# Performance work log

Measured on AMD Instinct MI355X. Metric: run time of the kernel, lower is better.

Reference implementation:

```python
import jax, jax.numpy as jnp
import numpy as np

COMMITMENT_COST = 0.25
DIST_SCALE = 400.0


def setup_inputs() -> dict:
    key = jax.random.key(0)
    ks = jax.random.split(key, 6)
    B, T, D, K = 64, 1024, 512, 512
    s = 1.0 / np.sqrt(D)
    return {
        "inputs": jax.random.normal(ks[0], (B, T, D), dtype=jnp.float32),
        "mean_W": jax.random.normal(ks[1], (D, D), dtype=jnp.float32) * s,
        "mean_b": jax.random.normal(ks[2], (D,), dtype=jnp.float32) * s,
        "logvar_W": jax.random.normal(ks[3], (D, K), dtype=jnp.float32) * s,
        "logvar_b": jax.random.normal(ks[4], (K,), dtype=jnp.float32) * s,
        "embedding": jax.random.normal(ks[5], (K, D), dtype=jnp.float32),
    }


def reference(inputs, mean_W, mean_b, logvar_W, logvar_b, embedding):
    sg = jax.lax.stop_gradient
    D = embedding.shape[1]
    flat = inputs.reshape(-1, D)                      # [N, D]
    x = flat @ mean_W + mean_b                        # mean_layer, [N, D]
    z_logvar = x @ logvar_W + logvar_b                # logvar_layer, [N, K]
    # squared euclidean distances to codebook, [N, K]
    distances = (
        jnp.sum(x * x, axis=1, keepdims=True)
        + jnp.sum(embedding * embedding, axis=1)
        - 2.0 * (x @ embedding.T)
    )
    smooth = jnp.exp(-2.0 * z_logvar)                 # 1/exp(logvar)^2
    d = distances / DIST_SCALE
    prob = jnp.exp(-d * (0.5 * smooth)) / jnp.sqrt(smooth)
    probs = prob / jnp.sum(prob, axis=1, keepdims=True)  # per-row normalize, [N, K]
    quantized = (probs @ embedding).reshape(inputs.shape)
    e_latent_loss = jnp.mean((sg(quantized) - inputs) ** 2)
    q_latent_loss = jnp.mean((quantized - sg(inputs)) ** 2)
    loss = q_latent_loss + COMMITMENT_COST * e_latent_loss
    quantized_st = inputs + sg(quantized - inputs)    # straight-through
    avg_probs = jnp.mean(probs, axis=0)
    perplexity = jnp.exp(-jnp.sum(avg_probs * jnp.log(avg_probs + 1e-10)))
    return loss, quantized_st, perplexity, probs
```

## Files before the change

### kernel.cpp

```cpp
#include <hip/hip_runtime.h>
#include <stdint.h>

#define DIMD 512
#define NROWS 65536
#define QOFF 1
#define PERPOFF 33554433
#define PROBSOFF 33554434
#define NELEM 33554432

typedef __attribute__((ext_vector_type(8))) short bf16x8;
typedef __attribute__((ext_vector_type(4))) short s16x4;
typedef __attribute__((ext_vector_type(4))) float f32x4;

__device__ __forceinline__ short f2bf(float x){
  uint32_t u = __builtin_bit_cast(uint32_t, x);
  uint32_t r = (u + 0x7fffu + ((u >> 16) & 1u)) >> 16;
  return (short)(uint16_t)r;
}
__device__ __forceinline__ float bf2f(short h){
  return __builtin_bit_cast(float, ((uint32_t)(uint16_t)h) << 16);
}

__device__ __forceinline__ int aoff(int row, int kc){
  return row * 512 + ((kc ^ (row & 7)) << 3);
}

__global__ __launch_bounds__(256) void k_convert_w(
    const float* __restrict__ meanW, const float* __restrict__ lvW, const float* __restrict__ emb,
    short* __restrict__ MWfh, short* __restrict__ MWfl,
    short* __restrict__ VWh, short* __restrict__ VWl,
    short* __restrict__ Eb, short* __restrict__ Et, float* __restrict__ enorm)
{
  int b = blockIdx.x;
  int tid = threadIdx.x;
  float esum = 0.f;
  for (int j = tid; j < 512; j += 256){
    long offB = ((long)(b >> 5) << 14) + j * 32 + (b & 31);
    float w = meanW[b * 512 + j];
    short h = f2bf(w); short l = f2bf(w - bf2f(h));
    MWfh[offB] = h; MWfl[offB] = l;
    float v = lvW[b * 512 + j];
    h = f2bf(v); l = f2bf(v - bf2f(h));
    VWh[offB] = h; VWl[offB] = l;
    float e = emb[b * 512 + j];
    short eh = f2bf(e);
    Eb[((long)(j >> 5) << 14) + b * 32 + (j & 31)] = eh;
    Et[offB] = eh;
    esum += e * e;
  }
  for (int o = 32; o >= 1; o >>= 1) esum += __shfl_xor(esum, o);
  __shared__ float red[4];
  if ((tid & 63) == 0) red[tid >> 6] = esum;
  __syncthreads();
  if (tid == 0) enorm[b] = red[0] + red[1] + red[2] + red[3];
}

__global__ __launch_bounds__(1024, 1) void k_fused(
    const float* __restrict__ inp,
    const short* __restrict__ MWfh, const short* __restrict__ MWfl,
    const short* __restrict__ VWh, const short* __restrict__ VWl,
    const short* __restrict__ Eb, const short* __restrict__ Et,
    const float* __restrict__ meanb, const float* __restrict__ lvb,
    const float* __restrict__ enorm,
    float* __restrict__ probs, float* __restrict__ qout,
    float* __restrict__ Pacc, float* __restrict__ lossacc)
{
  __shared__ short Ih[64 * 512];
  __shared__ short Il[64 * 512];
  __shared__ float rrM[16][64];
  __shared__ float rrS[16][64];

  const int tid = threadIdx.x;
  const int n0 = blockIdx.x * 64;
  const int lane = tid & 63, wid = tid >> 6;
  const int q = lane >> 4, m = lane & 15;
  const int c0 = wid * 32;

  int boff0 = (c0 + m) * 32 + q * 8;
  int boff1 = (c0 + 16 + m) * 32 + q * 8;

  {
    const float* inpb = inp + (long)n0 * 512;
#pragma unroll
    for (int it = 0; it < 8; ++it){
      int fid = tid + it * 1024;
      int row = fid >> 7, f = fid & 127;
      const float4 v = *(const float4*)(inpb + (long)fid * 4);
      short h0 = f2bf(v.x), h1 = f2bf(v.y), h2 = f2bf(v.z), h3 = f2bf(v.w);
      s16x4 hv; hv[0] = h0; hv[1] = h1; hv[2] = h2; hv[3] = h3;
      s16x4 lv;
      lv[0] = f2bf(v.x - bf2f(h0)); lv[1] = f2bf(v.y - bf2f(h1));
      lv[2] = f2bf(v.z - bf2f(h2)); lv[3] = f2bf(v.w - bf2f(h3));
      int ch = (f >> 1) ^ (row & 7);
      int addr = row * 512 + (ch << 3) + (f & 1) * 4;
      *(s16x4*)(Ih + addr) = hv;
      *(s16x4*)(Il + addr) = lv;
    }
  }
  __syncthreads();

  f32x4 accM[4][2];
#pragma unroll
  for (int i = 0; i < 4; i++)
#pragma unroll
    for (int j = 0; j < 2; j++)
#pragma unroll
      for (int r = 0; r < 4; r++) accM[i][j][r] = 0.f;
  {
    bf16x8 nbh0 = *(const bf16x8*)(MWfh + boff0);
    bf16x8 nbh1 = *(const bf16x8*)(MWfh + boff1);
    bf16x8 nbl0 = *(const bf16x8*)(MWfl + boff0);
    bf16x8 nbl1 = *(const bf16x8*)(MWfl + boff1);
#pragma unroll 2
    for (int ks = 0; ks < 16; ++ks){
      bf16x8 bh0 = nbh0, bh1 = nbh1, bl0 = nbl0, bl1 = nbl1;
      if (ks < 15){
        int o = (ks + 1) * 16384;
        nbh0 = *(const bf16x8*)(MWfh + o + boff0);
        nbh1 = *(const bf16x8*)(MWfh + o + boff1);
        nbl0 = *(const bf16x8*)(MWfl + o + boff0);
        nbl1 = *(const bf16x8*)(MWfl + o + boff1);
      }
      bf16x8 ah[4], al[4];
#pragma unroll
      for (int i = 0; i < 4; i++){
        int off = aoff(i * 16 + m, ks * 4 + q);
        ah[i] = *(const bf16x8*)(Ih + off);
        al[i] = *(const bf16x8*)(Il + off);
      }
#pragma unroll
      for (int i = 0; i < 4; i++){
        accM[i][0] = __builtin_amdgcn_mfma_f32_16x16x32_bf16(ah[i], bh0, accM[i][0], 0, 0, 0);
        accM[i][0] = __builtin_amdgcn_mfma_f32_16x16x32_bf16(ah[i], bl0, accM[i][0], 0, 0, 0);
        accM[i][0] = __builtin_amdgcn_mfma_f32_16x16x32_bf16(al[i], bh0, accM[i][0], 0, 0, 0);
        accM[i][1] = __builtin_amdgcn_mfma_f32_16x16x32_bf16(ah[i], bh1, accM[i][1], 0, 0, 0);
        accM[i][1] = __builtin_amdgcn_mfma_f32_16x16x32_bf16(ah[i], bl1, accM[i][1], 0, 0, 0);
        accM[i][1] = __builtin_amdgcn_mfma_f32_16x16x32_bf16(al[i], bh1, accM[i][1], 0, 0, 0);
      }
    }
  }
  __syncthreads();

  {
    float b0 = meanb[c0 + m], b1 = meanb[c0 + 16 + m];
#pragma unroll
    for (int i = 0; i < 4; i++)
#pragma unroll
      for (int r = 0; r < 4; r++){
        int row = i * 16 + q * 4 + r;
        float x0 = accM[i][0][r] + b0;
        float x1 = accM[i][1][r] + b1;
        int col0 = c0 + m, col1 = c0 + 16 + m;
        short h0 = f2bf(x0), h1 = f2bf(x1);
        int a0 = row * 512 + ((((col0 >> 3) ^ (row & 7)) << 3) | (col0 & 7));
        int a1 = row * 512 + ((((col1 >> 3) ^ (row & 7)) << 3) | (col1 & 7));
        Ih[a0] = h0; Il[a0] = f2bf(x0 - bf2f(h0));
        Ih[a1] = h1; Il[a1] = f2bf(x1 - bf2f(h1));
        float xn = x0 * x0 + x1 * x1;
        xn += __shfl_xor(xn, 1); xn += __shfl_xor(xn, 2);
        xn += __shfl_xor(xn, 4); xn += __shfl_xor(xn, 8);
        if (m == 0) rrS[wid][row] = xn;
      }
  }
  __syncthreads();

  float xnv[4][4];
  {
    float v = 0.f;
#pragma unroll
    for (int w = 0; w < 16; w++) v += rrS[w][lane];
#pragma unroll
    for (int i = 0; i < 4; i++)
#pragma unroll
      for (int r = 0; r < 4; r++) xnv[i][r] = __shfl(v, i * 16 + q * 4 + r);
  }

  f32x4 accZ[4][2];
#pragma unroll
  for (int i = 0; i < 4; i++)
#pragma unroll
    for (int j = 0; j < 2; j++)
#pragma unroll
      for (int r = 0; r < 4; r++) accZ[i][j][r] = 0.f;
  {
    bf16x8 nbh0 = *(const bf16x8*)(VWh + boff0);
    bf16x8 nbh1 = *(const bf16x8*)(VWh + boff1);
    bf16x8 nbl0 = *(const bf16x8*)(VWl + boff0);
    bf16x8 nbl1 = *(const bf16x8*)(VWl + boff1);
#pragma unroll 2
    for (int ks = 0; ks < 16; ++ks){
      bf16x8 bh0 = nbh0, bh1 = nbh1, bl0 = nbl0, bl1 = nbl1;
      if (ks < 15){
        int o = (ks + 1) * 16384;
        nbh0 = *(const bf16x8*)(VWh + o + boff0);
        nbh1 = *(const bf16x8*)(VWh + o + boff1);
        nbl0 = *(const bf16x8*)(VWl + o + boff0);
        nbl1 = *(const bf16x8*)(VWl + o + boff1);
      }
      bf16x8 ah[4], al[4];
#pragma unroll
      for (int i = 0; i < 4; i++){
        int off = aoff(i * 16 + m, ks * 4 + q);
        ah[i] = *(const bf16x8*)(Ih + off);
        al[i] = *(const bf16x8*)(Il + off);
      }
#pragma unroll
      for (int i = 0; i < 4; i++){
        accZ[i][0] = __builtin_amdgcn_mfma_f32_16x16x32_bf16(ah[i], bh0, accZ[i][0], 0, 0, 0);
        accZ[i][0] = __builtin_amdgcn_mfma_f32_16x16x32_bf16(ah[i], bl0, accZ[i][0], 0, 0, 0);
        accZ[i][0] = __builtin_amdgcn_mfma_f32_16x16x32_bf16(al[i], bh0, accZ[i][0], 0, 0, 0);
        accZ[i][1] = __builtin_amdgcn_mfma_f32_16x16x32_bf16(ah[i], bh1, accZ[i][1], 0, 0, 0);
        accZ[i][1] = __builtin_amdgcn_mfma_f32_16x16x32_bf16(ah[i], bl1, accZ[i][1], 0, 0, 0);
        accZ[i][1] = __builtin_amdgcn_mfma_f32_16x16x32_bf16(al[i], bh1, accZ[i][1], 0, 0, 0);
      }
    }
  }

  f32x4 accS[4][2];
#pragma unroll
  for (int i = 0; i < 4; i++)
#pragma unroll
    for (int j = 0; j < 2; j++)
#pragma unroll
      for (int r = 0; r < 4; r++) accS[i][j][r] = 0.f;
  {
    bf16x8 nb0 = *(const bf16x8*)(Eb + boff0);
    bf16x8 nb1 = *(const bf16x8*)(Eb + boff1);
#pragma unroll 2
    for (int ks = 0; ks < 16; ++ks){
      bf16x8 b0 = nb0, b1 = nb1;
      if (ks < 15){
        int o = (ks + 1) * 16384;
        nb0 = *(const bf16x8*)(Eb + o + boff0);
        nb1 = *(const bf16x8*)(Eb + o + boff1);
      }
      bf16x8 ah[4];
#pragma unroll
      for (int i = 0; i < 4; i++)
        ah[i] = *(const bf16x8*)(Ih + aoff(i * 16 + m, ks * 4 + q));
#pragma unroll
      for (int i = 0; i < 4; i++){
        accS[i][0] = __builtin_amdgcn_mfma_f32_16x16x32_bf16(ah[i], b0, accS[i][0], 0, 0, 0);
        accS[i][1] = __builtin_amdgcn_mfma_f32_16x16x32_bf16(ah[i], b1, accS[i][1], 0, 0, 0);
      }
    }
  }

  {
    float lvb0 = lvb[c0 + m], lvb1 = lvb[c0 + 16 + m];
    float en0 = enorm[c0 + m], en1 = enorm[c0 + 16 + m];
    const float inv800 = 0.5f / 400.0f;
#pragma unroll
    for (int i = 0; i < 4; i++)
#pragma unroll
      for (int r = 0; r < 4; r++){
        float z0 = accZ[i][0][r] + lvb0;
        float z1 = accZ[i][1][r] + lvb1;
        float sm0 = __expf(-2.f * z0), sm1 = __expf(-2.f * z1);
        accS[i][0][r] = z0 - inv800 * (xnv[i][r] + en0 - 2.f * accS[i][0][r]) * sm0;
        accS[i][1][r] = z1 - inv800 * (xnv[i][r] + en1 - 2.f * accS[i][1][r]) * sm1;
      }
  }

#pragma unroll
  for (int i = 0; i < 4; i++)
#pragma unroll
    for (int r = 0; r < 4; r++){
      float v = fmaxf(accS[i][0][r], accS[i][1][r]);
      v = fmaxf(v, __shfl_xor(v, 1));
      v = fmaxf(v, __shfl_xor(v, 2));
      v = fmaxf(v, __shfl_xor(v, 4));
      v = fmaxf(v, __shfl_xor(v, 8));
      if (m == 0) rrM[wid][i * 16 + q * 4 + r] = v;
    }
  __syncthreads();
  float mxf[4][4];
  {
    float v = rrM[0][lane];
#pragma unroll
    for (int w = 1; w < 16; w++) v = fmaxf(v, rrM[w][lane]);
#pragma unroll
    for (int i = 0; i < 4; i++)
#pragma unroll
      for (int r = 0; r < 4; r++) mxf[i][r] = __shfl(v, i * 16 + q * 4 + r);
  }

#pragma unroll
  for (int i = 0; i < 4; i++)
#pragma unroll
    for (int r = 0; r < 4; r++){
      float p0 = __expf(accS[i][0][r] - mxf[i][r]);
      float p1 = __expf(accS[i][1][r] - mxf[i][r]);
      accS[i][0][r] = p0; accS[i][1][r] = p1;
      float sacc = p0 + p1;
      sacc += __shfl_xor(sacc, 1);
      sacc += __shfl_xor(sacc, 2);
      sacc += __shfl_xor(sacc, 4);
      sacc += __shfl_xor(sacc, 8);
      if (m == 0) rrS[wid][i * 16 + q * 4 + r] = sacc;
    }
  __syncthreads();
  float smr[4][4];
  {
    float v = 0.f;
#pragma unroll
    for (int w = 0; w < 16; w++) v += rrS[w][lane];
#pragma unroll
    for (int i = 0; i < 4; i++)
#pragma unroll
      for (int r = 0; r < 4; r++) smr[i][r] = __shfl(v, i * 16 + q * 4 + r);
  }

  {
    float pj0 = 0.f, pj1 = 0.f;
#pragma unroll
    for (int i = 0; i < 4; i++)
#pragma unroll
      for (int r = 0; r < 4; r++){
        int row = i * 16 + q * 4 + r;
        long rowg = n0 + row;
        float inv = 1.0f / smr[i][r];
        float q0 = accS[i][0][r] * inv;
        float q1 = accS[i][1][r] * inv;
        int col0 = c0 + m, col1 = c0 + 16 + m;
        probs[rowg * 512 + col0] = q0;
        probs[rowg * 512 + col1] = q1;
        pj0 += q0; pj1 += q1;
        int a0 = row * 512 + ((((col0 >> 3) ^ (row & 7)) << 3) | (col0 & 7));
        int a1 = row * 512 + ((((col1 >> 3) ^ (row & 7)) << 3) | (col1 & 7));
        Ih[a0] = f2bf(q0);
        Ih[a1] = f2bf(q1);
      }
    pj0 += __shfl_xor(pj0, 16); pj0 += __shfl_xor(pj0, 32);
    pj1 += __shfl_xor(pj1, 16); pj1 += __shfl_xor(pj1, 32);
    if (lane < 16){
      atomicAdd(&Pacc[c0 + m], pj0);
      atomicAdd(&Pacc[c0 + 16 + m], pj1);
    }
  }
  __syncthreads();

  f32x4 accQ[4][2];
#pragma unroll
  for (int i = 0; i < 4; i++)
#pragma unroll
    for (int j = 0; j < 2; j++)
#pragma unroll
      for (int r = 0; r < 4; r++) accQ[i][j][r] = 0.f;
  {
    bf16x8 nb0 = *(const bf16x8*)(Et + boff0);
    bf16x8 nb1 = *(const bf16x8*)(Et + boff1);
#pragma unroll 2
    for (int ks = 0; ks < 16; ++ks){
      bf16x8 b0 = nb0, b1 = nb1;
      if (ks < 15){
        int o = (ks + 1) * 16384;
        nb0 = *(const bf16x8*)(Et + o + boff0);
        nb1 = *(const bf16x8*)(Et + o + boff1);
      }
      bf16x8 pa[4];
#pragma unroll
      for (int i = 0; i < 4; i++)
        pa[i] = *(const bf16x8*)(Ih + aoff(i * 16 + m, ks * 4 + q));
#pragma unroll
      for (int i = 0; i < 4; i++){
        accQ[i][0] = __builtin_amdgcn_mfma_f32_16x16x32_bf16(pa[i], b0, accQ[i][0], 0, 0, 0);
        accQ[i][1] = __builtin_amdgcn_mfma_f32_16x16x32_bf16(pa[i], b1, accQ[i][1], 0, 0, 0);
      }
    }
  }

  {
    float lsum = 0.f;
#pragma unroll
    for (int i = 0; i < 4; i++)
#pragma unroll
      for (int r = 0; r < 4; r++){
        long rowg = n0 + i * 16 + q * 4 + r;
        float q0 = accQ[i][0][r], q1 = accQ[i][1][r];
        long i0 = rowg * 512 + c0 + m;
        long i1 = rowg * 512 + c0 + 16 + m;
        qout[i0] = q0;
        qout[i1] = q1;
        float d0 = q0 - inp[i0], d1 = q1 - inp[i1];
        lsum += d0 * d0 + d1 * d1;
      }
    lsum += __shfl_xor(lsum, 32);
    lsum += __shfl_xor(lsum, 16);
    lsum += __shfl_xor(lsum, 8);
    lsum += __shfl_xor(lsum, 4);
    lsum += __shfl_xor(lsum, 2);
    lsum += __shfl_xor(lsum, 1);
    if (lane == 0) rrM[0][wid] = lsum;
  }
  __syncthreads();
  if (tid == 0){
    float t = 0.f;
#pragma unroll
    for (int w = 0; w < 16; w++) t += rrM[0][w];
    atomicAdd(lossacc, t);
  }
}

__global__ __launch_bounds__(256) void k_final(
    const float* __restrict__ Pacc, const float* __restrict__ lossacc, float* __restrict__ out)
{
  int tid = threadIdx.x;
  float h = 0.f;
  for (int k = tid; k < 512; k += 256){
    float a = Pacc[k] * (1.0f / 65536.0f);
    h += a * __logf(a + 1e-10f);
  }
  for (int o = 32; o >= 1; o >>= 1) h += __shfl_xor(h, o);
  __shared__ float red[4];
  if ((tid & 63) == 0) red[tid >> 6] = h;
  __syncthreads();
  if (tid == 0){
    float H = red[0] + red[1] + red[2] + red[3];
    out[0] = 1.25f * lossacc[0] * (1.0f / (float)NELEM);
    out[PERPOFF] = __expf(-H);
  }
}

extern "C" void kernel_launch(void* const* d_in, const int* in_sizes, int n_in,
                              void* d_out, int out_size, void* d_ws, size_t ws_size,
                              hipStream_t stream)
{
  const float* inp   = (const float*)d_in[0];
  const float* meanW = (const float*)d_in[1];
  const float* meanb = (const float*)d_in[2];
  const float* lvW   = (const float*)d_in[3];
  const float* lvb   = (const float*)d_in[4];
  const float* emb   = (const float*)d_in[5];
  float* out = (float*)d_out;

  char* w = (char*)d_ws;
  short* MWfh = (short*)w; w += 512 * 512 * 2;
  short* MWfl = (short*)w; w += 512 * 512 * 2;
  short* VWh  = (short*)w; w += 512 * 512 * 2;
  short* VWl  = (short*)w; w += 512 * 512 * 2;
  short* Eb   = (short*)w; w += 512 * 512 * 2;
  short* Et   = (short*)w; w += 512 * 512 * 2;
  float* enorm = (float*)w; w += 512 * 4;
  float* stats = (float*)w;
  float* Pacc    = stats;
  float* lossacc = stats + 512;

  hipMemsetAsync(stats, 0, (size_t)(512 + 16) * 4, stream);

  k_convert_w<<<512, 256, 0, stream>>>(meanW, lvW, emb, MWfh, MWfl, VWh, VWl, Eb, Et, enorm);
  k_fused<<<1024, 1024, 0, stream>>>(inp, MWfh, MWfl, VWh, VWl, Eb, Et, meanb, lvb, enorm,
                                     out + PROBSOFF, out + QOFF, Pacc, lossacc);
  k_final<<<1, 256, 0, stream>>>(Pacc, lossacc, out);
}
```

Before: 699.7 us.

## Use nontemporal loads/stores, raise MFMA wave priority, coalesce weight conversion

Inputs and outputs in the fused kernel are streamed through nontemporal loads and stores, so the large probs/quantized outputs and single-use inputs do not evict the reused weight tiles from cache. MFMA blocks are wrapped in s_setprio(1)/s_setprio(0) so that waves issuing matrix work get scheduling priority. The weight-conversion kernel is reorganized so its writes into the blocked layout are coalesced, and the codebook norm is now accumulated with atomics, which requires the memset to also zero enorm. The atomic norm changes summation order, and the priority hint may not help the schedule.

```diff
diff --git a/kernel.cpp b/kernel.cpp
--- a/kernel.cpp
+++ b/kernel.cpp
@@ -11,6 +11,7 @@
 typedef __attribute__((ext_vector_type(8))) short bf16x8;
 typedef __attribute__((ext_vector_type(4))) short s16x4;
 typedef __attribute__((ext_vector_type(4))) float f32x4;
+typedef __attribute__((ext_vector_type(4))) float f4v;
 
 __device__ __forceinline__ short f2bf(float x){
   uint32_t u = __builtin_bit_cast(uint32_t, x);
@@ -19,6 +20,16 @@
 }
 __device__ __forceinline__ float bf2f(short h){
   return __builtin_bit_cast(float, ((uint32_t)(uint16_t)h) << 16);
+}
+
+__device__ __forceinline__ f4v ntld4(const float* p){
+  return __builtin_nontemporal_load((const f4v*)p);
+}
+__device__ __forceinline__ float ntldf(const float* p){
+  return __builtin_nontemporal_load(p);
+}
+__device__ __forceinline__ void ntst(float* p, float v){
+  __builtin_nontemporal_store(v, p);
 }
 
 __device__ __forceinline__ int aoff(int row, int kc){
@@ -31,28 +42,28 @@
     short* __restrict__ VWh, short* __restrict__ VWl,
     short* __restrict__ Eb, short* __restrict__ Et, float* __restrict__ enorm)
 {
-  int b = blockIdx.x;
-  int tid = threadIdx.x;
-  float esum = 0.f;
-  for (int j = tid; j < 512; j += 256){
-    long offB = ((long)(b >> 5) << 14) + j * 32 + (b & 31);
-    float w = meanW[b * 512 + j];
-    short h = f2bf(w); short l = f2bf(w - bf2f(h));
-    MWfh[offB] = h; MWfl[offB] = l;
-    float v = lvW[b * 512 + j];
-    h = f2bf(v); l = f2bf(v - bf2f(h));
-    VWh[offB] = h; VWl[offB] = l;
-    float e = emb[b * 512 + j];
-    short eh = f2bf(e);
-    Eb[((long)(j >> 5) << 14) + b * 32 + (j & 31)] = eh;
-    Et[offB] = eh;
-    esum += e * e;
-  }
-  for (int o = 32; o >= 1; o >>= 1) esum += __shfl_xor(esum, o);
-  __shared__ float red[4];
-  if ((tid & 63) == 0) red[tid >> 6] = esum;
-  __syncthreads();
-  if (tid == 0) enorm[b] = red[0] + red[1] + red[2] + red[3];
+  int s = blockIdx.x >> 5;
+  int g = blockIdx.x & 31;
+  int t = threadIdx.x;
+  int kk = s * 32 + (t & 31);
+#pragma unroll
+  for (int it = 0; it < 2; ++it){
+    int R = g * 16 + (t >> 5) + it * 8;
+    long dst = (long)s * 16384 + R * 32 + (t & 31);
+    float w = meanW[(long)kk * 512 + R];
+    short h = f2bf(w);
+    MWfh[dst] = h; MWfl[dst] = f2bf(w - bf2f(h));
+    float v = lvW[(long)kk * 512 + R];
+    h = f2bf(v);
+    VWh[dst] = h; VWl[dst] = f2bf(v - bf2f(h));
+    Et[dst] = f2bf(emb[(long)kk * 512 + R]);
+    float e = emb[(long)R * 512 + kk];
+    Eb[dst] = f2bf(e);
+    float es = e * e;
+    es += __shfl_xor(es, 1); es += __shfl_xor(es, 2); es += __shfl_xor(es, 4);
+    es += __shfl_xor(es, 8); es += __shfl_xor(es, 16);
+    if ((t & 31) == 0) atomicAdd(&enorm[R], es);
+  }
 }
 
 __global__ __launch_bounds__(1024, 1) void k_fused(
@@ -85,12 +96,12 @@
     for (int it = 0; it < 8; ++it){
       int fid = tid + it * 1024;
       int row = fid >> 7, f = fid & 127;
-      const float4 v = *(const float4*)(inpb + (long)fid * 4);
-      short h0 = f2bf(v.x), h1 = f2bf(v.y), h2 = f2bf(v.z), h3 = f2bf(v.w);
+      const f4v v = ntld4(inpb + (long)fid * 4);
+      short h0 = f2bf(v[0]), h1 = f2bf(v[1]), h2 = f2bf(v[2]), h3 = f2bf(v[3]);
       s16x4 hv; hv[0] = h0; hv[1] = h1; hv[2] = h2; hv[3] = h3;
       s16x4 lv;
-      lv[0] = f2bf(v.x - bf2f(h0)); lv[1] = f2bf(v.y - bf2f(h1));
-      lv[2] = f2bf(v.z - bf2f(h2)); lv[3] = f2bf(v.w - bf2f(h3));
+      lv[0] = f2bf(v[0] - bf2f(h0)); lv[1] = f2bf(v[1] - bf2f(h1));
+      lv[2] = f2bf(v[2] - bf2f(h2)); lv[3] = f2bf(v[3] - bf2f(h3));
       int ch = (f >> 1) ^ (row & 7);
       int addr = row * 512 + (ch << 3) + (f & 1) * 4;
       *(s16x4*)(Ih + addr) = hv;
@@ -128,6 +139,7 @@
         ah[i] = *(const bf16x8*)(Ih + off);
         al[i] = *(const bf16x8*)(Il + off);
       }
+      __builtin_amdgcn_s_setprio(1);
 #pragma unroll
       for (int i = 0; i < 4; i++){
         accM[i][0] = __builtin_amdgcn_mfma_f32_16x16x32_bf16(ah[i], bh0, accM[i][0], 0, 0, 0);
@@ -137,6 +149,7 @@
         accM[i][1] = __builtin_amdgcn_mfma_f32_16x16x32_bf16(ah[i], bl1, accM[i][1], 0, 0, 0);
         accM[i][1] = __builtin_amdgcn_mfma_f32_16x16x32_bf16(al[i], bh1, accM[i][1], 0, 0, 0);
       }
+      __builtin_amdgcn_s_setprio(0);
     }
   }
   __syncthreads();
@@ -204,6 +217,7 @@
         ah[i] = *(const bf16x8*)(Ih + off);
         al[i] = *(const bf16x8*)(Il + off);
       }
+      __builtin_amdgcn_s_setprio(1);
 #pragma unroll
       for (int i = 0; i < 4; i++){
         accZ[i][0] = __builtin_amdgcn_mfma_f32_16x16x32_bf16(ah[i], bh0, accZ[i][0], 0, 0, 0);
@@ -213,6 +227,7 @@
         accZ[i][1] = __builtin_amdgcn_mfma_f32_16x16x32_bf16(ah[i], bl1, accZ[i][1], 0, 0, 0);
         accZ[i][1] = __builtin_amdgcn_mfma_f32_16x16x32_bf16(al[i], bh1, accZ[i][1], 0, 0, 0);
       }
+      __builtin_amdgcn_s_setprio(0);
     }
   }
 
@@ -238,11 +253,13 @@
 #pragma unroll
       for (int i = 0; i < 4; i++)
         ah[i] = *(const bf16x8*)(Ih + aoff(i * 16 + m, ks * 4 + q));
+      __builtin_amdgcn_s_setprio(1);
 #pragma unroll
       for (int i = 0; i < 4; i++){
         accS[i][0] = __builtin_amdgcn_mfma_f32_16x16x32_bf16(ah[i], b0, accS[i][0], 0, 0, 0);
         accS[i][1] = __builtin_amdgcn_mfma_f32_16x16x32_bf16(ah[i], b1, accS[i][1], 0, 0, 0);
       }
+      __builtin_amdgcn_s_setprio(0);
     }
   }
 
@@ -323,8 +340,8 @@
         float q0 = accS[i][0][r] * inv;
         float q1 = accS[i][1][r] * inv;
         int col0 = c0 + m, col1 = c0 + 16 + m;
-        probs[rowg * 512 + col0] = q0;
-        probs[rowg * 512 + col1] = q1;
+        ntst(&probs[rowg * 512 + col0], q0);
+        ntst(&probs[rowg * 512 + col1], q1);
         pj0 += q0; pj1 += q1;
         int a0 = row * 512 + ((((col0 >> 3) ^ (row & 7)) << 3) | (col0 & 7));
         int a1 = row * 512 + ((((col1 >> 3) ^ (row & 7)) << 3) | (col1 & 7));
@@ -362,11 +379,13 @@
 #pragma unroll
       for (int i = 0; i < 4; i++)
         pa[i] = *(const bf16x8*)(Ih + aoff(i * 16 + m, ks * 4 + q));
+      __builtin_amdgcn_s_setprio(1);
 #pragma unroll
       for (int i = 0; i < 4; i++){
         accQ[i][0] = __builtin_amdgcn_mfma_f32_16x16x32_bf16(pa[i], b0, accQ[i][0], 0, 0, 0);
         accQ[i][1] = __builtin_amdgcn_mfma_f32_16x16x32_bf16(pa[i], b1, accQ[i][1], 0, 0, 0);
       }
+      __builtin_amdgcn_s_setprio(0);
     }
   }
 
@@ -380,9 +399,9 @@
         float q0 = accQ[i][0][r], q1 = accQ[i][1][r];
         long i0 = rowg * 512 + c0 + m;
         long i1 = rowg * 512 + c0 + 16 + m;
-        qout[i0] = q0;
-        qout[i1] = q1;
-        float d0 = q0 - inp[i0], d1 = q1 - inp[i1];
+        ntst(&qout[i0], q0);
+        ntst(&qout[i1], q1);
+        float d0 = q0 - ntldf(&inp[i0]), d1 = q1 - ntldf(&inp[i1]);
         lsum += d0 * d0 + d1 * d1;
       }
     lsum += __shfl_xor(lsum, 32);
@@ -446,7 +465,7 @@
   float* Pacc    = stats;
   float* lossacc = stats + 512;
 
-  hipMemsetAsync(stats, 0, (size_t)(512 + 16) * 4, stream);
+  hipMemsetAsync(enorm, 0, (size_t)(512 + 512 + 16) * 4, stream);
 
   k_convert_w<<<512, 256, 0, stream>>>(meanW, lvW, emb, MWfh, MWfl, VWh, VWl, Eb, Et, enorm);
   k_fused<<<1024, 1024, 0, stream>>>(inp, MWfh, MWfl, VWh, VWl, Eb, Et, meanb, lvb, enorm,
```

Result: slower. 768.4 us (+9.8%).
